# Performance work log

Hardware: AMD Instinct MI355X
Metric: run time of the kernel (lower is better)

## Reference

```python
import jax, jax.numpy as jnp
import numpy as np

B, D = 8, 128
CH = [1, 2, 4, 8, 16, 32, 64]
STRIDES = [1, 2, 2, 2, 2, 2]
EPS = 1e-5


def setup_inputs() -> dict:
    key = jax.random.key(0)
    ks = jax.random.split(key, 8)
    inp = {
        'x_feats': jax.random.normal(ks[0], (B, D, D, D, 1), jnp.float32),
        'x_mask': jax.random.randint(ks[1], (B, D, D, D, 1), 0, 2).astype(jnp.int32),
    }
    for i in range(6):
        cin, cout = CH[i], CH[i + 1]
        inp[f'w{i}'] = jax.random.normal(ks[2 + i], (3, 3, 3, cin, cout), jnp.float32) * (1.0 / np.sqrt(27.0 * cin))
        inp[f'g{i}'] = jnp.ones((cout,), jnp.float32)
        inp[f'b{i}'] = jnp.zeros((cout,), jnp.float32)
    return inp


def _conv(x, w, stride):
    # x: [B,D,D,D,Cin], w: [3,3,3,Cin,Cout]; SAME-style pad=1 so output index p gathers stride*p + {-1,0,1}
    return jax.lax.conv_general_dilated(
        x, w, (stride,) * 3, [(1, 1)] * 3,
        dimension_numbers=('NDHWC', 'DHWIO', 'NDHWC'))


def _down_mask(m):
    # ME strided coord map: out coord p active iff any input coord c with floor(c/2)==p is active
    return jax.lax.reduce_window(m, 0.0, jax.lax.max,
                                 (1, 2, 2, 2, 1), (1, 2, 2, 2, 1), 'VALID')


def _bn_relu(x, m, g, b):
    # batch-norm over ACTIVE voxels only (x is already zero at inactive sites)
    cnt = jnp.maximum(jnp.sum(m), 1.0)
    mean = jnp.sum(x, axis=(0, 1, 2, 3)) / cnt            # [C]
    var = jnp.sum(x * x, axis=(0, 1, 2, 3)) / cnt - mean * mean
    y = (x - mean) * (g * jax.lax.rsqrt(var + EPS)) + b
    return jnp.maximum(y, 0.0) * m


def _forward(x_feats, x_mask, ws, gs, bs):
    m = x_mask.astype(x_feats.dtype)
    x = x_feats * m
    for i in range(6):
        x = _conv(x, ws[i], STRIDES[i])
        if STRIDES[i] == 2:
            m = _down_mask(m)
        x = x * m  # zero values at inactive output coords (sparse tensor semantics)
        x = _bn_relu(x, m, gs[i], bs[i])
    # sparse max pooling k=3 s=2: max over active inputs in footprint 2p+{-1,0,1}
    neg = jnp.asarray(-jnp.inf, x.dtype)
    filled = jnp.where(m > 0, x, neg)
    pooled = jax.lax.reduce_window(filled, neg, jax.lax.max,
                                   (1, 3, 3, 3, 1), (1, 2, 2, 2, 1),
                                   [(0, 0), (1, 1), (1, 1), (1, 1), (0, 0)])
    mo = _down_mask(m)
    return jnp.where(mo > 0, pooled, 0.0)  # [B, 2, 2, 2, 64]


def reference(x_feats, x_mask, w0, w1, w2, w3, w4, w5,
              g0, g1, g2, g3, g4, g5, b0, b1, b2, b3, b4, b5):
    ws = [w0, w1, w2, w3, w4, w5]
    gs = [g0, g1, g2, g3, g4, g5]
    bs = [b0, b1, b2, b3, b4, b5]
    return _forward(x_feats, x_mask, ws, gs, bs)
```

## Files before the change

kernel.cpp:

```cpp
#include <hip/hip_runtime.h>
#include <hip/hip_bf16.h>
#include <stdint.h>

#define DEV __device__ __forceinline__

constexpr int BATCH = 8;

constexpr int il2(int n) { return (n <= 1) ? 0 : 1 + il2(n / 2); }

DEV float ldy(const float* p, int i) { return p[i]; }
DEV float ldy(const __hip_bfloat16* p, int i) { return __bfloat162float(p[i]); }
DEV void sty(float* p, size_t i, float v) { p[i] = v; }
DEV void sty(__hip_bfloat16* p, size_t i, float v) { p[i] = __float2bfloat16(v); }

DEV uint32_t f2bf(float v) {
  __hip_bfloat16 h = __float2bfloat16(v);
  return (uint32_t)*reinterpret_cast<uint16_t*>(&h);
}
DEV float bflo(uint32_t u) {
  uint32_t t = u << 16;
  float f;
  __builtin_memcpy(&f, &t, 4);
  return f;
}
DEV float bfhi(uint32_t u) {
  uint32_t t = u & 0xffff0000u;
  float f;
  __builtin_memcpy(&f, &t, 4);
  return f;
}
constexpr uint32_t NEGINF_BF = 0xFF80u;
DEV int xswz(int o, int nwg) { return (o & 7) * (nwg >> 3) + (o >> 3); }

__global__ __launch_bounds__(256) void maskA_k(const int* __restrict__ msk,
                                               uint8_t* __restrict__ m0,
                                               uint8_t* __restrict__ m1,
                                               uint8_t* __restrict__ m2) {
  __shared__ uint8_t t0[32768];
  __shared__ uint8_t t1[4096];
  int blk = blockIdx.x;
  int bx = (blk & 3) * 32, by = ((blk >> 2) & 3) * 32, bz = ((blk >> 4) & 3) * 32, b = blk >> 6;
  int tid = threadIdx.x;
  for (int g = tid; g < 8192; g += 256) {
    int gx4 = (g & 7) * 4, gy = (g >> 3) & 31, gz = g >> 8;
    int gidx = ((b * 128 + bz + gz) * 128 + by + gy) * 128 + bx + gx4;
    int4 v = *(const int4*)(msk + gidx);
    uint32_t o = (v.x ? 1u : 0u) | (v.y ? 256u : 0u) | (v.z ? 65536u : 0u) | (v.w ? 16777216u : 0u);
    ((uint32_t*)t0)[g] = o;
    ((uint32_t*)m0)[gidx >> 2] = o;
  }
  __syncthreads();
  for (int j = tid; j < 4096; j += 256) {
    int ox = j & 15, oy = (j >> 4) & 15, oz = j >> 8;
    uint32_t act = 0;
#pragma unroll
    for (int dz = 0; dz < 2; dz++)
#pragma unroll
      for (int dy = 0; dy < 2; dy++)
        act |= *(const uint16_t*)&t0[(2 * oz + dz) * 1024 + (2 * oy + dy) * 32 + 2 * ox];
    uint8_t vv = act ? 1 : 0;
    t1[j] = vv;
    m1[((b * 64 + bz / 2 + oz) * 64 + by / 2 + oy) * 64 + bx / 2 + ox] = vv;
  }
  __syncthreads();
  for (int j = tid; j < 512; j += 256) {
    int ox = j & 7, oy = (j >> 3) & 7, oz = j >> 6;
    uint32_t act = 0;
#pragma unroll
    for (int dz = 0; dz < 2; dz++)
#pragma unroll
      for (int dy = 0; dy < 2; dy++)
        act |= *(const uint16_t*)&t1[(2 * oz + dz) * 256 + (2 * oy + dy) * 16 + 2 * ox];
    m2[((b * 32 + bz / 4 + oz) * 32 + by / 4 + oy) * 32 + bx / 4 + ox] = act ? 1 : 0;
  }
}

__global__ __launch_bounds__(1024) void maskB_k(const uint8_t* __restrict__ m2,
                                                uint8_t* __restrict__ m3,
                                                uint8_t* __restrict__ m4,
                                                uint8_t* __restrict__ m5,
                                                uint8_t* __restrict__ m6) {
  __shared__ uint8_t t3[32768];
  __shared__ uint8_t t4[4096];
  __shared__ uint8_t t5[512];
  int tid = threadIdx.x;
  for (int j = tid; j < 32768; j += 1024) {
    int ox = j & 15, oy = (j >> 4) & 15, oz = (j >> 8) & 15, b = j >> 12;
    uint32_t act = 0;
#pragma unroll
    for (int dz = 0; dz < 2; dz++)
#pragma unroll
      for (int dy = 0; dy < 2; dy++)
        act |= *(const uint16_t*)&m2[((b * 32 + 2 * oz + dz) * 32 + 2 * oy + dy) * 32 + 2 * ox];
    uint8_t v = act ? 1 : 0;
    t3[j] = v;
    m3[j] = v;
  }
  __syncthreads();
  for (int j = tid; j < 4096; j += 1024) {
    int ox = j & 7, oy = (j >> 3) & 7, oz = (j >> 6) & 7, b = j >> 9;
    uint32_t act = 0;
#pragma unroll
    for (int dz = 0; dz < 2; dz++)
#pragma unroll
      for (int dy = 0; dy < 2; dy++)
        act |= *(const uint16_t*)&t3[((b * 16 + 2 * oz + dz) * 16 + 2 * oy + dy) * 16 + 2 * ox];
    uint8_t v = act ? 1 : 0;
    t4[j] = v;
    m4[j] = v;
  }
  __syncthreads();
  if (tid < 512) {
    int j = tid;
    int ox = j & 3, oy = (j >> 2) & 3, oz = (j >> 4) & 3, b = j >> 6;
    uint32_t act = 0;
#pragma unroll
    for (int dz = 0; dz < 2; dz++)
#pragma unroll
      for (int dy = 0; dy < 2; dy++)
        act |= *(const uint16_t*)&t4[((b * 8 + 2 * oz + dz) * 8 + 2 * oy + dy) * 8 + 2 * ox];
    uint8_t v = act ? 1 : 0;
    t5[j] = v;
    m5[j] = v;
  }
  __syncthreads();
  if (tid < 64) {
    int j = tid;
    int ox = j & 1, oy = (j >> 1) & 1, oz = (j >> 2) & 1, b = j >> 3;
    uint32_t act = 0;
#pragma unroll
    for (int dz = 0; dz < 2; dz++)
#pragma unroll
      for (int dy = 0; dy < 2; dy++)
        act |= *(const uint16_t*)&t5[((b * 4 + 2 * oz + dz) * 4 + 2 * oy + dy) * 4 + 2 * ox];
    m6[j] = act ? 1 : 0;
  }
}

__global__ __launch_bounds__(512) void conv0_k(const float* __restrict__ x,
                                               const uint8_t* __restrict__ m0,
                                               const float* __restrict__ w,
                                               __hip_bfloat16* __restrict__ y0,
                                               float* __restrict__ partials) {
  constexpr int NSITE = 5832;
  constexpr int ROUNDS = 12;
  __shared__ float sx[NSITE];
  __shared__ float sm[8][5];
  int blk = xswz(blockIdx.x, 4096);
  int tx0 = (blk & 7) * 16, ty0 = ((blk >> 3) & 7) * 16, tz0 = ((blk >> 6) & 7) * 16, b = blk >> 9;
  int tid = threadIdx.x;

  float xv[ROUNDS];
  uint32_t mv[ROUNDS];
#pragma unroll
  for (int r = 0; r < ROUNDS; r++) {
    unsigned i = tid + r * 512;
    int sz = i / 324;
    int rr = i - sz * 324;
    int sy = rr / 18;
    int sxx = rr - sy * 18;
    int gz = tz0 + sz - 1, gy = ty0 + sy - 1, gx = tx0 + sxx - 1;
    bool in = (i < NSITE) & ((unsigned)gz < 128u) & ((unsigned)gy < 128u) & ((unsigned)gx < 128u);
    int gi = in ? ((b * 128 + gz) * 128 + gy) * 128 + gx : 0;
    uint32_t mraw = m0[gi];
    float xraw = x[gi];
    mv[r] = in ? mraw : 0u;
    xv[r] = xraw;
  }
#pragma unroll
  for (int r = 0; r < ROUNDS; r++) {
    unsigned i = tid + r * 512;
    if (i < NSITE) sx[i] = mv[r] ? xv[r] : 0.f;
  }
  __syncthreads();

  int tc = tid & 7, tb = (tid >> 3) & 7, ta = tid >> 6;
  int lx = tc * 2, ly = tb * 2, lz = ta * 2;

  uint32_t mm[2][2];
#pragma unroll
  for (int oz = 0; oz < 2; oz++)
#pragma unroll
    for (int oy = 0; oy < 2; oy++) {
      int z = tz0 + lz + oz, y = ty0 + ly + oy, xx = tx0 + lx;
      mm[oz][oy] = *(const uint16_t*)(m0 + ((b * 128 + z) * 128 + y) * 128 + xx);
    }

  float rg[4][4][4];
#pragma unroll
  for (int dz = 0; dz < 4; dz++)
#pragma unroll
    for (int dy = 0; dy < 4; dy++)
#pragma unroll
      for (int dx = 0; dx < 4; dx += 2) {
        float2 v = *(const float2*)&sx[(lz + dz) * 324 + (ly + dy) * 18 + lx + dx];
        rg[dz][dy][dx] = v.x;
        rg[dz][dy][dx + 1] = v.y;
      }

  float acc[2][2][2][2];
#pragma unroll
  for (int oz = 0; oz < 2; oz++)
#pragma unroll
    for (int oy = 0; oy < 2; oy++)
#pragma unroll
      for (int ox = 0; ox < 2; ox++)
        acc[oz][oy][ox][0] = acc[oz][oy][ox][1] = 0.f;

#pragma unroll
  for (int dz = 0; dz < 3; dz++)
#pragma unroll
    for (int dy = 0; dy < 3; dy++)
#pragma unroll
      for (int dx = 0; dx < 3; dx++) {
        float w0 = w[((dz * 3 + dy) * 3 + dx) * 2];
        float w1 = w[((dz * 3 + dy) * 3 + dx) * 2 + 1];
#pragma unroll
        for (int oz = 0; oz < 2; oz++)
#pragma unroll
          for (int oy = 0; oy < 2; oy++)
#pragma unroll
            for (int ox = 0; ox < 2; ox++) {
              float s = rg[oz + dz][oy + dy][ox + dx];
              acc[oz][oy][ox][0] = fmaf(s, w0, acc[oz][oy][ox][0]);
              acc[oz][oy][ox][1] = fmaf(s, w1, acc[oz][oy][ox][1]);
            }
      }

  float s0 = 0.f, q0 = 0.f, s1 = 0.f, q1 = 0.f;
  int cnt = 0;
#pragma unroll
  for (int oz = 0; oz < 2; oz++)
#pragma unroll
    for (int oy = 0; oy < 2; oy++) {
      int z = tz0 + lz + oz, y = ty0 + ly + oy, xx = tx0 + lx;
      int vo = ((b * 128 + z) * 128 + y) * 128 + xx;
      uint32_t m2b = mm[oz][oy];
      uint2 st;
      if (m2b & 0xff) {
        st.x = f2bf(acc[oz][oy][0][0]) | (f2bf(acc[oz][oy][0][1]) << 16);
        s0 += acc[oz][oy][0][0];
        q0 += acc[oz][oy][0][0] * acc[oz][oy][0][0];
        s1 += acc[oz][oy][0][1];
        q1 += acc[oz][oy][0][1] * acc[oz][oy][0][1];
        cnt++;
      } else {
        st.x = NEGINF_BF | (NEGINF_BF << 16);
      }
      if (m2b >> 8) {
        st.y = f2bf(acc[oz][oy][1][0]) | (f2bf(acc[oz][oy][1][1]) << 16);
        s0 += acc[oz][oy][1][0];
        q0 += acc[oz][oy][1][0] * acc[oz][oy][1][0];
        s1 += acc[oz][oy][1][1];
        q1 += acc[oz][oy][1][1] * acc[oz][oy][1][1];
        cnt++;
      } else {
        st.y = NEGINF_BF | (NEGINF_BF << 16);
      }
      ((uint2*)y0)[vo >> 1] = st;
    }
  float cf = (float)cnt;
#pragma unroll
  for (int off = 32; off >= 1; off >>= 1) {
    s0 += __shfl_xor(s0, off);
    q0 += __shfl_xor(q0, off);
    s1 += __shfl_xor(s1, off);
    q1 += __shfl_xor(q1, off);
    cf += __shfl_xor(cf, off);
  }
  int wave = tid >> 6;
  if ((tid & 63) == 0) {
    sm[wave][0] = s0;
    sm[wave][1] = q0;
    sm[wave][2] = s1;
    sm[wave][3] = q1;
    sm[wave][4] = cf;
  }
  __syncthreads();
  if (tid < 5) {
    float t = 0.f;
#pragma unroll
    for (int wv = 0; wv < 8; wv++) t += sm[wv][tid];
    partials[blk * 5 + tid] = t;
  }
}

template <int Din, int Cin, int Cout, int TZ, typename Tin, typename Tout>
__global__ __launch_bounds__(512) void conv_tile_k(const Tin* __restrict__ yin,
                                                   const uint8_t* __restrict__ mo,
                                                   const float* __restrict__ ssin,
                                                   const float* __restrict__ w,
                                                   Tout* __restrict__ yout,
                                                   float* __restrict__ partials) {
  static_assert(sizeof(Tin) == 2 && (Cin == 2 || Cin == 4), "bf16 input only");
  constexpr int Dout = Din / 2;
  constexpr int NT = 64 * TZ;
  constexpr int IZ = 2 * TZ + 1;
  constexpr int NS = 289 * IZ;
  constexpr int ROUNDS = (NS + NT - 1) / NT;
  constexpr int TXN = Dout / 8;
  constexpr int TZN = Dout / TZ;
  constexpr int LTX = il2(TXN);
  constexpr int LTZ = il2(TZN);
  constexpr int NWG = TXN * TXN * TZN * BATCH;
  constexpr int REC = 2 * Cout + 1;
  __shared__ float sx[NS * Cin];
  __shared__ float sm[TZ][REC];

  int tid = threadIdx.x;
  int blk = xswz(blockIdx.x, NWG);
  int tx0 = (blk & (TXN - 1)) * 8;
  int ty0 = ((blk >> LTX) & (TXN - 1)) * 8;
  int tz0 = ((blk >> (2 * LTX)) & (TZN - 1)) * TZ;
  int b = blk >> (2 * LTX + LTZ);

  float sc[Cin], sh[Cin];
#pragma unroll
  for (int ci = 0; ci < Cin; ci++) {
    sc[ci] = ssin[2 * ci];
    sh[ci] = ssin[2 * ci + 1];
  }

  int ox = 2 * tx0 - 1, oy = 2 * ty0 - 1, oz = 2 * tz0 - 1;
  uint32_t xv0[ROUNDS], xv1[ROUNDS];
  uint32_t inbits = 0;
#pragma unroll
  for (int r = 0; r < ROUNDS; r++) {
    unsigned i = tid + r * NT;
    int sz = i / 289;
    int r2 = i - sz * 289;
    int sy = r2 / 17;
    int sxx = r2 - sy * 17;
    int gz = oz + sz, gy = oy + sy, gx = ox + sxx;
    bool in = (i < NS) & ((unsigned)gz < (unsigned)Din) & ((unsigned)gy < (unsigned)Din) &
              ((unsigned)gx < (unsigned)Din);
    int gi = in ? ((b * Din + gz) * Din + gy) * Din + gx : 0;
    if (in) inbits |= (1u << r);
    if constexpr (Cin == 2) {
      xv0[r] = *(const uint32_t*)((const uint16_t*)yin + (size_t)gi * 2);
    } else {
      uint2 t = *(const uint2*)((const uint16_t*)yin + (size_t)gi * 4);
      xv0[r] = t.x;
      xv1[r] = t.y;
    }
  }
#pragma unroll
  for (int r = 0; r < ROUNDS; r++) {
    unsigned i = tid + r * NT;
    if (i >= NS) continue;
    bool in = (inbits >> r) & 1u;
    if constexpr (Cin == 2) {
      float f0 = fmaxf(fmaf(bflo(xv0[r]), sc[0], sh[0]), 0.f);
      float f1 = fmaxf(fmaf(bfhi(xv0[r]), sc[1], sh[1]), 0.f);
      sx[i * 2] = in ? f0 : 0.f;
      sx[i * 2 + 1] = in ? f1 : 0.f;
    } else {
      float f0 = fmaxf(fmaf(bflo(xv0[r]), sc[0], sh[0]), 0.f);
      float f1 = fmaxf(fmaf(bfhi(xv0[r]), sc[1], sh[1]), 0.f);
      float f2 = fmaxf(fmaf(bflo(xv1[r]), sc[2], sh[2]), 0.f);
      float f3 = fmaxf(fmaf(bfhi(xv1[r]), sc[3], sh[3]), 0.f);
      sx[i * 4] = in ? f0 : 0.f;
      sx[i * 4 + 1] = in ? f1 : 0.f;
      sx[i * 4 + 2] = in ? f2 : 0.f;
      sx[i * 4 + 3] = in ? f3 : 0.f;
    }
  }
  __syncthreads();

  int tc = tid & 7, tb = (tid >> 3) & 7, ta = tid >> 6;
  int lx = tc, ly = tb, lz = ta;
  int vo = ((b * Dout + tz0 + lz) * Dout + ty0 + ly) * Dout + tx0 + lx;
  bool act = mo[vo] != 0;
  float acc[Cout];
#pragma unroll
  for (int co = 0; co < Cout; co++) acc[co] = 0.f;
  if (act) {
    int base = ((2 * lz) * 289 + (2 * ly) * 17 + (2 * lx)) * Cin;
#pragma unroll
    for (int dz = 0; dz < 3; dz++)
#pragma unroll
      for (int dy = 0; dy < 3; dy++)
#pragma unroll
        for (int dx = 0; dx < 3; dx++) {
          int off = base + (dz * 289 + dy * 17 + dx) * Cin;
          const float* wp = w + ((dz * 3 + dy) * 3 + dx) * Cin * Cout;
#pragma unroll
          for (int ci = 0; ci < Cin; ci++) {
            float s = sx[off + ci];
#pragma unroll
            for (int co = 0; co < Cout; co++)
              acc[co] = fmaf(s, wp[ci * Cout + co], acc[co]);
          }
        }
  }
  {
    uint32_t pk[Cout / 2];
    if (act) {
#pragma unroll
      for (int k = 0; k < Cout / 2; k++) pk[k] = f2bf(acc[2 * k]) | (f2bf(acc[2 * k + 1]) << 16);
    } else {
#pragma unroll
      for (int k = 0; k < Cout / 2; k++) pk[k] = NEGINF_BF | (NEGINF_BF << 16);
    }
    if constexpr (Cout == 4)
      *(uint2*)((uint16_t*)yout + (size_t)vo * 4) = *(uint2*)pk;
    else if constexpr (Cout == 8)
      *(uint4*)((uint16_t*)yout + (size_t)vo * 8) = *(uint4*)pk;
    else {
#pragma unroll
      for (int k = 0; k < Cout / 2; k++)
        *((uint32_t*)yout + (size_t)vo * (Cout / 2) + k) = pk[k];
    }
  }
  unsigned long long bal = __ballot(act);
  int wave = tid >> 6, lane = tid & 63;
#pragma unroll
  for (int co = 0; co < Cout; co++) {
    float s = acc[co], q = acc[co] * acc[co];
#pragma unroll
    for (int off = 32; off >= 1; off >>= 1) {
      s += __shfl_xor(s, off);
      q += __shfl_xor(q, off);
    }
    if (lane == 0) {
      sm[wave][2 * co] = s;
      sm[wave][2 * co + 1] = q;
    }
  }
  if (lane == 0) sm[wave][2 * Cout] = (float)__popcll(bal);
  __syncthreads();
  if (tid < REC) {
    float t = 0.f;
#pragma unroll
    for (int wv = 0; wv < TZ; wv++) t += sm[wv][tid];
    partials[(size_t)blk * REC + tid] = t;
  }
}

template <int Din, int Cin, int Cout, typename Tin, typename Tout>
__global__ __launch_bounds__(256) void conv_s2_k(const Tin* __restrict__ yin,
                                                 const uint8_t* __restrict__ mo,
                                                 const float* __restrict__ ssin,
                                                 const float* __restrict__ w,
                                                 Tout* __restrict__ yout,
                                                 float* __restrict__ partials) {
  constexpr int Dout = Din / 2;
  constexpr int LD = il2(Dout);
  constexpr int LC = il2(Cout);
  constexpr int REC = 2 * Cout + 1;
  int tid = threadIdx.x;
  int lin = blockIdx.x * 256 + tid;
  int co = lin & (Cout - 1);
  int v = lin >> LC;
  int x = v & (Dout - 1);
  int y = (v >> LD) & (Dout - 1);
  int z = (v >> (2 * LD)) & (Dout - 1);
  int b = v >> (3 * LD);
  bool act = mo[v] != 0;
  float acc = 0.f;
  if (act) {
    for (int dz = 0; dz < 3; dz++) {
      int iz = 2 * z + dz - 1;
      if ((unsigned)iz >= (unsigned)Din) continue;
      for (int dy = 0; dy < 3; dy++) {
        int iy = 2 * y + dy - 1;
        if ((unsigned)iy >= (unsigned)Din) continue;
        for (int dx = 0; dx < 3; dx++) {
          int ix = 2 * x + dx - 1;
          if ((unsigned)ix >= (unsigned)Din) continue;
          int gi = ((b * Din + iz) * Din + iy) * Din + ix;
          const float* wp = w + ((dz * 3 + dy) * 3 + dx) * Cin * Cout + co;
          float f[Cin];
          if constexpr (sizeof(Tin) == 2 && Cin == 8) {
            uint4 rr = *(const uint4*)((const uint16_t*)yin + (size_t)gi * 8);
            f[0] = bflo(rr.x);
            f[1] = bfhi(rr.x);
            f[2] = bflo(rr.y);
            f[3] = bfhi(rr.y);
            f[4] = bflo(rr.z);
            f[5] = bfhi(rr.z);
            f[6] = bflo(rr.w);
            f[7] = bfhi(rr.w);
          } else {
            const Tin* yp = yin + (size_t)gi * Cin;
#pragma unroll
            for (int ci = 0; ci < Cin; ci++) f[ci] = ldy(yp, ci);
          }
#pragma unroll
          for (int ci = 0; ci < Cin; ci++) {
            float val = fmaxf(fmaf(f[ci], ssin[2 * ci], ssin[2 * ci + 1]), 0.f);
            acc = fmaf(val, wp[ci * Cout], acc);
          }
        }
      }
    }
  }
  sty(yout, (size_t)lin, act ? acc : -INFINITY);
  float s = acc, q = acc * acc;
#pragma unroll
  for (int off = 32; off >= Cout; off >>= 1) {
    s += __shfl_xor(s, off);
    q += __shfl_xor(q, off);
  }
  unsigned long long bal = __ballot(act && co == 0);
  __shared__ float sm[4][REC];
  int wave = tid >> 6, lane = tid & 63;
  if (lane < Cout) {
    sm[wave][2 * lane] = s;
    sm[wave][2 * lane + 1] = q;
  }
  if (lane == 0) sm[wave][2 * Cout] = (float)__popcll(bal);
  __syncthreads();
  if (tid < REC)
    partials[(size_t)blockIdx.x * REC + tid] = sm[0][tid] + sm[1][tid] + sm[2][tid] + sm[3][tid];
}

template <int Cout>
__global__ __launch_bounds__(256) void stats_k(const float* __restrict__ partials, int nblocks,
                                               const float* __restrict__ g,
                                               const float* __restrict__ bb,
                                               float* __restrict__ ss) {
  constexpr int REC = 2 * Cout + 1;
  int c = blockIdx.x, tid = threadIdx.x;
  float s = 0.f, q = 0.f, n = 0.f;
  for (int i = tid; i < nblocks; i += 256) {
    const float* p = partials + (size_t)i * REC;
    s += p[2 * c];
    q += p[2 * c + 1];
    n += p[2 * Cout];
  }
  __shared__ float S[256], Q[256], N[256];
  S[tid] = s;
  Q[tid] = q;
  N[tid] = n;
  __syncthreads();
  for (int st = 128; st > 0; st >>= 1) {
    if (tid < st) {
      S[tid] += S[tid + st];
      Q[tid] += Q[tid + st];
      N[tid] += N[tid + st];
    }
    __syncthreads();
  }
  if (tid == 0) {
    float cnt = fmaxf(N[0], 1.f);
    float mean = S[0] / cnt;
    float var = Q[0] / cnt - mean * mean;
    float scale = g[c] * rsqrtf(var + 1e-5f);
    ss[2 * c] = scale;
    ss[2 * c + 1] = bb[c] - mean * scale;
  }
}

__global__ __launch_bounds__(512) void pool_stats_k(const float* __restrict__ y5,
                                                    const uint8_t* __restrict__ m6,
                                                    const float* __restrict__ partials,
                                                    const float* __restrict__ g,
                                                    const float* __restrict__ bb,
                                                    float* __restrict__ out) {
  __shared__ float ssc[64], ssh[64];
  int b = blockIdx.x, tid = threadIdx.x;
  if (tid < 64) {
    float s = 0.f, q = 0.f, n = 0.f;
    for (int i = 0; i < 128; i++) {
      const float* p = partials + i * 129;
      s += p[2 * tid];
      q += p[2 * tid + 1];
      n += p[128];
    }
    float cnt = fmaxf(n, 1.f);
    float mean = s / cnt;
    float var = q / cnt - mean * mean;
    float scale = g[tid] * rsqrtf(var + 1e-5f);
    ssc[tid] = scale;
    ssh[tid] = bb[tid] - mean * scale;
  }
  __syncthreads();
  int c = tid & 63, s = tid >> 6;
  int qx = s & 1, qy = (s >> 1) & 1, qz = (s >> 2) & 1;
  int ov = ((b * 2 + qz) * 2 + qy) * 2 + qx;
  float scale = ssc[c], shift = ssh[c];
  float mx = 0.f;
  for (int dz = 0; dz < 3; dz++) {
    int iz = 2 * qz + dz - 1;
    if ((unsigned)iz >= 4u) continue;
    for (int dy = 0; dy < 3; dy++) {
      int iy = 2 * qy + dy - 1;
      if ((unsigned)iy >= 4u) continue;
      for (int dx = 0; dx < 3; dx++) {
        int ix = 2 * qx + dx - 1;
        if ((unsigned)ix >= 4u) continue;
        int gi = ((b * 4 + iz) * 4 + iy) * 4 + ix;
        float val = fmaxf(fmaf(y5[gi * 64 + c], scale, shift), 0.f);
        mx = fmaxf(mx, val);
      }
    }
  }
  out[ov * 64 + c] = m6[ov] ? mx : 0.f;
}

extern "C" void kernel_launch(void* const* d_in, const int* in_sizes, int n_in,
                              void* d_out, int out_size, void* d_ws, size_t ws_size,
                              hipStream_t stream) {
  const float* x = (const float*)d_in[0];
  const int* msk = (const int*)d_in[1];
  const float *w[6], *g[6], *bb[6];
  for (int i = 0; i < 6; i++) {
    w[i] = (const float*)d_in[2 + 3 * i];
    g[i] = (const float*)d_in[3 + 3 * i];
    bb[i] = (const float*)d_in[4 + 3 * i];
  }

  char* ws = (char*)d_ws;
  size_t o = 0;
  auto A = [&](size_t bytes) -> char* {
    char* p = ws + o;
    o = (o + bytes + 255) & ~(size_t)255;
    return p;
  };
  __hip_bfloat16* y0 = (__hip_bfloat16*)A(33554432 * 2);
  __hip_bfloat16* y1 = (__hip_bfloat16*)A(8388608 * 2);
  __hip_bfloat16* y2 = (__hip_bfloat16*)A(2097152 * 2);
  float* y3 = (float*)A(2097152);
  float* y4 = (float*)A(524288);
  float* y5 = (float*)A(131072);
  uint8_t* m0 = (uint8_t*)A(16777216);
  uint8_t* m1 = (uint8_t*)A(2097152);
  uint8_t* m2 = (uint8_t*)A(262144);
  uint8_t* m3 = (uint8_t*)A(32768);
  uint8_t* m4 = (uint8_t*)A(4096);
  uint8_t* m5 = (uint8_t*)A(512);
  uint8_t* m6 = (uint8_t*)A(64);
  float* part = (float*)A(2 << 20);
  float* ss = (float*)A(4096);
  if (o > ws_size) return;

  maskA_k<<<512, 256, 0, stream>>>(msk, m0, m1, m2);
  maskB_k<<<1, 1024, 0, stream>>>(m2, m3, m4, m5, m6);

  conv0_k<<<4096, 512, 0, stream>>>(x, m0, w[0], y0, part);
  stats_k<2><<<2, 256, 0, stream>>>(part, 4096, g[0], bb[0], ss + 0);
  conv_tile_k<128, 2, 4, 8, __hip_bfloat16, __hip_bfloat16>
      <<<4096, 512, 0, stream>>>(y0, m1, ss + 0, w[1], y1, part);
  stats_k<4><<<4, 256, 0, stream>>>(part, 4096, g[1], bb[1], ss + 128);
  conv_tile_k<64, 4, 8, 4, __hip_bfloat16, __hip_bfloat16>
      <<<1024, 256, 0, stream>>>(y1, m2, ss + 128, w[2], y2, part);
  stats_k<8><<<8, 256, 0, stream>>>(part, 1024, g[2], bb[2], ss + 256);
  conv_s2_k<32, 8, 16, __hip_bfloat16, float>
      <<<2048, 256, 0, stream>>>(y2, m3, ss + 256, w[3], y3, part);
  stats_k<16><<<16, 256, 0, stream>>>(part, 2048, g[3], bb[3], ss + 384);
  conv_s2_k<16, 16, 32, float, float>
      <<<512, 256, 0, stream>>>(y3, m4, ss + 384, w[4], y4, part);
  stats_k<32><<<32, 256, 0, stream>>>(part, 512, g[4], bb[4], ss + 512);
  conv_s2_k<8, 32, 64, float, float>
      <<<128, 256, 0, stream>>>(y4, m5, ss + 512, w[5], y5, part);
  pool_stats_k<<<8, 512, 0, stream>>>(y5, m6, part, g[5], bb[5], (float*)d_out);
}
```

Baseline: 252.4 us.

## Halve conv0 and conv1 tile depth, stream z-planes, raise occupancy bounds

conv0 now uses 256-thread blocks with 8-deep z tiles, so it launches twice as many workgroups. It packs the per-round mask into one bitfield and streams one z-plane at a time from LDS instead of holding a 4x4x4 register cube. conv_tile_k's launch bounds now request 8 blocks per CU, and the first strided conv uses TZ=4 with 8192 blocks. The aim is lower register and LDS pressure and higher occupancy, at the cost of more halo reloads per output and more partial sums for the stats kernels to reduce.

```diff
diff --git a/kernel.cpp b/kernel.cpp
--- a/kernel.cpp
+++ b/kernel.cpp
@@ -137,24 +137,25 @@
   }
 }
 
-__global__ __launch_bounds__(512) void conv0_k(const float* __restrict__ x,
-                                               const uint8_t* __restrict__ m0,
-                                               const float* __restrict__ w,
-                                               __hip_bfloat16* __restrict__ y0,
-                                               float* __restrict__ partials) {
-  constexpr int NSITE = 5832;
-  constexpr int ROUNDS = 12;
+__global__ __launch_bounds__(256, 8) void conv0_k(const float* __restrict__ x,
+                                                  const uint8_t* __restrict__ m0,
+                                                  const float* __restrict__ w,
+                                                  __hip_bfloat16* __restrict__ y0,
+                                                  float* __restrict__ partials) {
+  constexpr int NSITE = 3240;
+  constexpr int ROUNDS = 13;
   __shared__ float sx[NSITE];
-  __shared__ float sm[8][5];
-  int blk = xswz(blockIdx.x, 4096);
-  int tx0 = (blk & 7) * 16, ty0 = ((blk >> 3) & 7) * 16, tz0 = ((blk >> 6) & 7) * 16, b = blk >> 9;
+  __shared__ float sm[4][5];
+  int blk = xswz(blockIdx.x, 8192);
+  int tx0 = (blk & 7) * 16, ty0 = ((blk >> 3) & 7) * 16, tz0 = ((blk >> 6) & 15) * 8,
+      b = blk >> 10;
   int tid = threadIdx.x;
 
   float xv[ROUNDS];
-  uint32_t mv[ROUNDS];
+  uint32_t mbits = 0;
 #pragma unroll
   for (int r = 0; r < ROUNDS; r++) {
-    unsigned i = tid + r * 512;
+    unsigned i = tid + r * 256;
     int sz = i / 324;
     int rr = i - sz * 324;
     int sy = rr / 18;
@@ -164,13 +165,13 @@
     int gi = in ? ((b * 128 + gz) * 128 + gy) * 128 + gx : 0;
     uint32_t mraw = m0[gi];
     float xraw = x[gi];
-    mv[r] = in ? mraw : 0u;
+    if (in && mraw) mbits |= (1u << r);
     xv[r] = xraw;
   }
 #pragma unroll
   for (int r = 0; r < ROUNDS; r++) {
-    unsigned i = tid + r * 512;
-    if (i < NSITE) sx[i] = mv[r] ? xv[r] : 0.f;
+    unsigned i = tid + r * 256;
+    if (i < NSITE) sx[i] = ((mbits >> r) & 1u) ? xv[r] : 0.f;
   }
   __syncthreads();
 
@@ -186,18 +187,6 @@
       mm[oz][oy] = *(const uint16_t*)(m0 + ((b * 128 + z) * 128 + y) * 128 + xx);
     }
 
-  float rg[4][4][4];
-#pragma unroll
-  for (int dz = 0; dz < 4; dz++)
-#pragma unroll
-    for (int dy = 0; dy < 4; dy++)
-#pragma unroll
-      for (int dx = 0; dx < 4; dx += 2) {
-        float2 v = *(const float2*)&sx[(lz + dz) * 324 + (ly + dy) * 18 + lx + dx];
-        rg[dz][dy][dx] = v.x;
-        rg[dz][dy][dx + 1] = v.y;
-      }
-
   float acc[2][2][2][2];
 #pragma unroll
   for (int oz = 0; oz < 2; oz++)
@@ -208,24 +197,37 @@
         acc[oz][oy][ox][0] = acc[oz][oy][ox][1] = 0.f;
 
 #pragma unroll
-  for (int dz = 0; dz < 3; dz++)
-#pragma unroll
-    for (int dy = 0; dy < 3; dy++)
-#pragma unroll
-      for (int dx = 0; dx < 3; dx++) {
-        float w0 = w[((dz * 3 + dy) * 3 + dx) * 2];
-        float w1 = w[((dz * 3 + dy) * 3 + dx) * 2 + 1];
-#pragma unroll
-        for (int oz = 0; oz < 2; oz++)
+  for (int p = 0; p < 4; p++) {
+    float pl[4][4];
+#pragma unroll
+    for (int yy = 0; yy < 4; yy++)
+#pragma unroll
+      for (int xx2 = 0; xx2 < 4; xx2 += 2) {
+        float2 v = *(const float2*)&sx[(lz + p) * 324 + (ly + yy) * 18 + lx + xx2];
+        pl[yy][xx2] = v.x;
+        pl[yy][xx2 + 1] = v.y;
+      }
+#pragma unroll
+    for (int oz = 0; oz < 2; oz++) {
+      int dz = p - oz;
+      if (dz < 0 || dz > 2) continue;
+#pragma unroll
+      for (int dy = 0; dy < 3; dy++)
+#pragma unroll
+        for (int dx = 0; dx < 3; dx++) {
+          float w0 = w[((dz * 3 + dy) * 3 + dx) * 2];
+          float w1 = w[((dz * 3 + dy) * 3 + dx) * 2 + 1];
 #pragma unroll
           for (int oy = 0; oy < 2; oy++)
 #pragma unroll
             for (int ox = 0; ox < 2; ox++) {
-              float s = rg[oz + dz][oy + dy][ox + dx];
+              float s = pl[oy + dy][ox + dx];
               acc[oz][oy][ox][0] = fmaf(s, w0, acc[oz][oy][ox][0]);
               acc[oz][oy][ox][1] = fmaf(s, w1, acc[oz][oy][ox][1]);
             }
-      }
+        }
+    }
+  }
 
   float s0 = 0.f, q0 = 0.f, s1 = 0.f, q1 = 0.f;
   int cnt = 0;
@@ -280,18 +282,18 @@
   if (tid < 5) {
     float t = 0.f;
 #pragma unroll
-    for (int wv = 0; wv < 8; wv++) t += sm[wv][tid];
+    for (int wv = 0; wv < 4; wv++) t += sm[wv][tid];
     partials[blk * 5 + tid] = t;
   }
 }
 
 template <int Din, int Cin, int Cout, int TZ, typename Tin, typename Tout>
-__global__ __launch_bounds__(512) void conv_tile_k(const Tin* __restrict__ yin,
-                                                   const uint8_t* __restrict__ mo,
-                                                   const float* __restrict__ ssin,
-                                                   const float* __restrict__ w,
-                                                   Tout* __restrict__ yout,
-                                                   float* __restrict__ partials) {
+__global__ __launch_bounds__(64 * TZ, 8) void conv_tile_k(const Tin* __restrict__ yin,
+                                                          const uint8_t* __restrict__ mo,
+                                                          const float* __restrict__ ssin,
+                                                          const float* __restrict__ w,
+                                                          Tout* __restrict__ yout,
+                                                          float* __restrict__ partials) {
   static_assert(sizeof(Tin) == 2 && (Cin == 2 || Cin == 4), "bf16 input only");
   constexpr int Dout = Din / 2;
   constexpr int NT = 64 * TZ;
@@ -638,11 +640,11 @@
   maskA_k<<<512, 256, 0, stream>>>(msk, m0, m1, m2);
   maskB_k<<<1, 1024, 0, stream>>>(m2, m3, m4, m5, m6);
 
-  conv0_k<<<4096, 512, 0, stream>>>(x, m0, w[0], y0, part);
-  stats_k<2><<<2, 256, 0, stream>>>(part, 4096, g[0], bb[0], ss + 0);
-  conv_tile_k<128, 2, 4, 8, __hip_bfloat16, __hip_bfloat16>
-      <<<4096, 512, 0, stream>>>(y0, m1, ss + 0, w[1], y1, part);
-  stats_k<4><<<4, 256, 0, stream>>>(part, 4096, g[1], bb[1], ss + 128);
+  conv0_k<<<8192, 256, 0, stream>>>(x, m0, w[0], y0, part);
+  stats_k<2><<<2, 256, 0, stream>>>(part, 8192, g[0], bb[0], ss + 0);
+  conv_tile_k<128, 2, 4, 4, __hip_bfloat16, __hip_bfloat16>
+      <<<8192, 256, 0, stream>>>(y0, m1, ss + 0, w[1], y1, part);
+  stats_k<4><<<4, 256, 0, stream>>>(part, 8192, g[1], bb[1], ss + 128);
   conv_tile_k<64, 4, 8, 4, __hip_bfloat16, __hip_bfloat16>
       <<<1024, 256, 0, stream>>>(y1, m2, ss + 128, w[2], y2, part);
   stats_k<8><<<8, 256, 0, stream>>>(part, 1024, g[2], bb[2], ss + 256);
```

Result: slower. 342.0 us (+35.5%).
